# Optimization experiments

Hardware: AMD Instinct MI355X
Metric: run time of the kernel (lower is better)

The kernel has to match this reference:

```python
import jax, jax.numpy as jnp
import numpy as np

HIDDEN = 2048
NUM_HEADS = 16
NUM_KV_HEADS = 4
HEAD_DIM = HIDDEN // NUM_HEADS  # 128
ROPE_THETA = 1000000.0
B, S = 2, 2048


def setup_inputs() -> dict:
    key = jax.random.key(0)
    ks = jax.random.split(key, 10)
    sc = 0.02
    return {
        "hidden_states": jax.random.normal(ks[0], (B, S, HIDDEN), jnp.float32),
        "position_ids": jnp.broadcast_to(jnp.arange(S, dtype=jnp.int32), (B, S)),
        "Wq": jax.random.normal(ks[1], (HIDDEN, NUM_HEADS * HEAD_DIM), jnp.float32) * sc,
        "bq": jnp.zeros((NUM_HEADS * HEAD_DIM,), jnp.float32),
        "Wk": jax.random.normal(ks[2], (HIDDEN, NUM_KV_HEADS * HEAD_DIM), jnp.float32) * sc,
        "bk": jnp.zeros((NUM_KV_HEADS * HEAD_DIM,), jnp.float32),
        "Wv": jax.random.normal(ks[3], (HIDDEN, NUM_KV_HEADS * HEAD_DIM), jnp.float32) * sc,
        "bv": jnp.zeros((NUM_KV_HEADS * HEAD_DIM,), jnp.float32),
        "Wo": jax.random.normal(ks[4], (NUM_HEADS * HEAD_DIM, HIDDEN), jnp.float32) * sc,
        "bo": jnp.zeros((HIDDEN,), jnp.float32),
    }


def _rope_cos_sin(position_ids, dtype):
    # inv_freq: [head_dim/2]
    inv_freq = 1.0 / (ROPE_THETA ** (jnp.arange(0, HEAD_DIM, 2, dtype=jnp.float32) / HEAD_DIM))
    freqs = position_ids.astype(jnp.float32)[:, :, None] * inv_freq[None, None, :]  # [B,S,d/2]
    emb = jnp.concatenate([freqs, freqs], axis=-1)  # [B,S,d]
    return jnp.cos(emb).astype(dtype), jnp.sin(emb).astype(dtype)


def _rotate_half(x):
    h = x.shape[-1] // 2
    return jnp.concatenate([-x[..., h:], x[..., :h]], axis=-1)


def _attention(hidden_states, position_ids, Wq, bq, Wk, bk, Wv, bv, Wo, bo):
    bsz, q_len, _ = hidden_states.shape
    q = (hidden_states @ Wq + bq).reshape(bsz, q_len, NUM_HEADS, HEAD_DIM).transpose(0, 2, 1, 3)
    k = (hidden_states @ Wk + bk).reshape(bsz, q_len, NUM_KV_HEADS, HEAD_DIM).transpose(0, 2, 1, 3)
    v = (hidden_states @ Wv + bv).reshape(bsz, q_len, NUM_KV_HEADS, HEAD_DIM).transpose(0, 2, 1, 3)

    cos, sin = _rope_cos_sin(position_ids, hidden_states.dtype)
    cos = cos[:, None, :, :]  # [B,1,S,d]
    sin = sin[:, None, :, :]
    q = q * cos + _rotate_half(q) * sin
    k = k * cos + _rotate_half(k) * sin

    # repeat_kv (GQA): [B,kvh,S,d] -> [B,H,S,d]
    n_rep = NUM_HEADS // NUM_KV_HEADS
    k = jnp.repeat(k, n_rep, axis=1)
    v = jnp.repeat(v, n_rep, axis=1)

    scale = 1.0 / jnp.sqrt(jnp.array(HEAD_DIM, hidden_states.dtype))
    scores = jnp.einsum('bhqd,bhkd->bhqk', q, k) * scale  # [B,H,S,S]
    causal = jnp.tril(jnp.ones((q_len, q_len), bool))
    scores = jnp.where(causal[None, None], scores, jnp.finfo(scores.dtype).min)
    probs = jax.nn.softmax(scores.astype(jnp.float32), axis=-1).astype(hidden_states.dtype)
    attn = jnp.einsum('bhqk,bhkd->bhqd', probs, v)
    attn = attn.transpose(0, 2, 1, 3).reshape(bsz, q_len, HIDDEN)
    return attn @ Wo + bo


def reference(hidden_states, position_ids, Wq, bq, Wk, bk, Wv, bv, Wo, bo):
    return _attention(hidden_states, position_ids, Wq, bq, Wk, bk, Wv, bv, Wo, bo)
```

## Files before the change

kernel.cpp:

```cpp
#include <hip/hip_runtime.h>
#include <cmath>

#define HIDDEN 2048
#define NH 16
#define NKV 4
#define HD 128
#define SEQ 2048
#define BATCH 2

typedef unsigned short ushort_t;
typedef short bf16x8 __attribute__((ext_vector_type(8)));
typedef float f32x4 __attribute__((ext_vector_type(4)));
typedef ushort_t u16x4 __attribute__((ext_vector_type(4)));

__device__ __forceinline__ ushort_t f2bf(float f) {
    union { float f; unsigned int u; } v; v.f = f;
    unsigned int r = v.u + 0x7fffu + ((v.u >> 16) & 1u);
    return (ushort_t)(r >> 16);
}
__device__ __forceinline__ ushort_t f2bf_trunc(float f) {
    union { float f; unsigned int u; } v; v.f = f;
    return (ushort_t)(v.u >> 16);
}

__device__ __forceinline__ f32x4 mfma16(bf16x8 a, bf16x8 b, f32x4 c) {
    return __builtin_amdgcn_mfma_f32_16x16x32_bf16(a, b, c, 0, 0, 0);
}

__device__ __forceinline__ void load_lds16(const void* g, void* l) {
    __builtin_amdgcn_global_load_lds((const __attribute__((address_space(1))) unsigned int*)g,
                                     (__attribute__((address_space(3))) unsigned int*)l,
                                     16, 0, 0);
}


__global__ __launch_bounds__(256) void convert_x(const float* __restrict__ x,
                                                 ushort_t* __restrict__ xb, int n4) {
    int g = blockIdx.x * 256 + threadIdx.x;
    if (g >= n4) return;
    float4 v = ((const float4*)x)[g];
    u16x4 o;
    o[0] = f2bf(v.x); o[1] = f2bf(v.y); o[2] = f2bf(v.z); o[3] = f2bf(v.w);
    ((u16x4*)xb)[g] = o;
}

__global__ __launch_bounds__(256) void transpose_w(const float* __restrict__ W,
                                                   ushort_t* __restrict__ WT, int K, int N) {
    __shared__ ushort_t T[64][72];
    const int n0 = blockIdx.x * 64, k0 = blockIdx.y * 64;
    const int t = threadIdx.x;
    for (int idx = t; idx < 64 * 16; idx += 256) {
        int r = idx >> 4, c4 = (idx & 15) << 2;
        float4 v = *(const float4*)&W[(size_t)(k0 + r) * N + n0 + c4];
        T[r][c4 + 0] = f2bf(v.x); T[r][c4 + 1] = f2bf(v.y);
        T[r][c4 + 2] = f2bf(v.z); T[r][c4 + 3] = f2bf(v.w);
    }
    __syncthreads();
    for (int idx = t; idx < 64 * 16; idx += 256) {
        int n = idx >> 4, kg = (idx & 15) << 2;
        u16x4 o;
        o[0] = T[kg + 0][n]; o[1] = T[kg + 1][n];
        o[2] = T[kg + 2][n]; o[3] = T[kg + 3][n];
        *(u16x4*)&WT[(size_t)(n0 + n) * K + k0 + kg] = o;
    }
}

template <int MODE>
__global__ __launch_bounds__(256) void gemm_bt(const ushort_t* __restrict__ A,
                                               const ushort_t* __restrict__ Bt,
                                               const float* __restrict__ bias,
                                               const float* __restrict__ bias2,
                                               void* __restrict__ out,
                                               void* __restrict__ out2,
                                               int M, int N, int K,
                                               const int* __restrict__ posids) {
    __shared__ __align__(16) ushort_t As[2][128 * 32];
    __shared__ __align__(16) ushort_t Bs[2][128 * 32];
    const int tid = threadIdx.x;
    const int w = tid >> 6, lane = tid & 63, quad = lane >> 4, l16 = lane & 15;
    const int m0 = blockIdx.y * 128, n0 = blockIdx.x * 128;

    f32x4 acc[2][8];
    for (int i = 0; i < 2; i++)
        for (int j = 0; j < 8; j++)
            for (int e = 0; e < 4; e++) acc[i][j][e] = 0.0f;

    const int rr = lane >> 2;
    const int gc8 = (((lane & 3) ^ ((lane >> 3) & 3)) << 3);
    const ushort_t* Ag = A + (size_t)(m0 + w * 32 + rr) * K + gc8;
    const ushort_t* Bg = Bt + (size_t)(n0 + w * 32 + rr) * K + gc8;
    ushort_t* Al0 = &As[0][(w * 32) * 32];
    ushort_t* Bl0 = &Bs[0][(w * 32) * 32];

    auto stage = [&](int bi, int k0) {
        const ushort_t* ag = Ag + k0;
        const ushort_t* bg = Bg + k0;
        ushort_t* la = Al0 + bi * 128 * 32;
        ushort_t* lb = Bl0 + bi * 128 * 32;
        load_lds16(ag, la);
        load_lds16(ag + (size_t)16 * K, la + 512);
        load_lds16(bg, lb);
        load_lds16(bg + (size_t)16 * K, lb + 512);
    };

    const int nk = K >> 5;
    const int rsw = ((l16 >> 1) & 3);
    stage(0, 0);
    __syncthreads();

    for (int ki = 0; ki < nk; ki++) {
        const int cur = ki & 1;
        if (ki + 1 < nk) stage(cur ^ 1, (ki + 1) << 5);
        const ushort_t* Ab = As[cur];
        const ushort_t* Bb = Bs[cur];
        bf16x8 af[2];
#pragma unroll
        for (int i = 0; i < 2; i++)
            af[i] = *(const bf16x8*)&Ab[(w * 32 + i * 16 + l16) * 32 + (quad ^ rsw) * 8];
#pragma unroll
        for (int j = 0; j < 8; j++) {
            bf16x8 bf = *(const bf16x8*)&Bb[(j * 16 + l16) * 32 + (quad ^ rsw) * 8];
#pragma unroll
            for (int i = 0; i < 2; i++) acc[i][j] = mfma16(af[i], bf, acc[i][j]);
        }
        __syncthreads();
    }

    if (MODE == 0) {
        float* O = (float*)out;
#pragma unroll
        for (int i = 0; i < 2; i++)
#pragma unroll
            for (int r = 0; r < 4; r++) {
                int row = m0 + w * 32 + i * 16 + quad * 4 + r;
#pragma unroll
                for (int j = 0; j < 8; j++) {
                    int col = n0 + j * 16 + l16;
                    O[(size_t)row * N + col] = acc[i][j][r] + bias[col];
                }
            }
    } else if (MODE == 1) {
        ushort_t* O = (ushort_t*)out;
        const int h = n0 >> 7;
        const float scale = 0.08838834764831845f;
#pragma unroll
        for (int i = 0; i < 2; i++)
#pragma unroll
            for (int r = 0; r < 4; r++) {
                int row = m0 + w * 32 + i * 16 + quad * 4 + r;
                int b = row >> 11, s = row & (SEQ - 1);
                float pos = (float)posids[row];
                size_t obase = ((size_t)(b * NH + h) * SEQ + s) * HD;
#pragma unroll
                for (int j = 0; j < 4; j++) {
                    int dl = j * 16 + l16;
                    float x1 = acc[i][j][r] + bias[n0 + dl];
                    float x2 = acc[i][j + 4][r] + bias[n0 + dl + 64];
                    float ang = pos * __expf(-0.21586735246819178f * (float)dl);
                    float sn, cs;
                    __sincosf(ang, &sn, &cs);
                    O[obase + dl]      = f2bf((x1 * cs - x2 * sn) * scale);
                    O[obase + dl + 64] = f2bf((x2 * cs + x1 * sn) * scale);
                }
            }
    } else {
        if (n0 < 512) {
            ushort_t* O = (ushort_t*)out;
            const int h = n0 >> 7;
#pragma unroll
            for (int i = 0; i < 2; i++)
#pragma unroll
                for (int r = 0; r < 4; r++) {
                    int row = m0 + w * 32 + i * 16 + quad * 4 + r;
                    int b = row >> 11, s = row & (SEQ - 1);
                    float pos = (float)posids[row];
                    size_t obase = ((size_t)(b * NKV + h) * SEQ + s) * HD;
#pragma unroll
                    for (int j = 0; j < 4; j++) {
                        int dl = j * 16 + l16;
                        float x1 = acc[i][j][r] + bias[n0 + dl];
                        float x2 = acc[i][j + 4][r] + bias[n0 + dl + 64];
                        float ang = pos * __expf(-0.21586735246819178f * (float)dl);
                        float sn, cs;
                        __sincosf(ang, &sn, &cs);
                        O[obase + dl]      = f2bf(x1 * cs - x2 * sn);
                        O[obase + dl + 64] = f2bf(x2 * cs + x1 * sn);
                    }
                }
        } else {
            ushort_t* O = (ushort_t*)out2;
            const int n0v = n0 - 512;
            const int h = n0v >> 7;
#pragma unroll
            for (int i = 0; i < 2; i++)
#pragma unroll
                for (int r = 0; r < 4; r++) {
                    int row = m0 + w * 32 + i * 16 + quad * 4 + r;
                    int b = row >> 11, s = row & (SEQ - 1);
#pragma unroll
                    for (int j = 0; j < 8; j++) {
                        int d = (n0v & 127) + j * 16 + l16;
                        float v = acc[i][j][r] + bias2[n0v + j * 16 + l16];
                        O[((size_t)(b * NKV + h) * HD + d) * SEQ + s] = f2bf(v);
                    }
                }
        }
    }
}

__global__ __launch_bounds__(256) void flash(const ushort_t* __restrict__ Qr,
                                             const ushort_t* __restrict__ Kr,
                                             const ushort_t* __restrict__ Vt,
                                             ushort_t* __restrict__ Attn) {
    __shared__ __align__(16) ushort_t Ksh[2 * 4 * 64 * 32];
    __shared__ __align__(16) ushort_t Vsh[2 * 2 * 128 * 32];
    __shared__ __align__(16) ushort_t Ps[4 * 16 * 72];
    const int tid = threadIdx.x;
    const int w = tid >> 6, lane = tid & 63, quad = lane >> 4, l16 = lane & 15;
    const int x = blockIdx.x, h = blockIdx.y, b = blockIdx.z;
    const int qt = b ? x : (gridDim.x - 1 - x);
    const int q0 = qt * 128;
    const int nkt = 2 * qt + 2;
    const int hkv = h >> 2;
    const ushort_t* Kg = Kr + ((size_t)(b * NKV + hkv) * SEQ) * HD;
    const ushort_t* Vg = Vt + ((size_t)(b * NKV + hkv) * HD) * SEQ;

    const int p = lane >> 2;
    const int gc8 = (((lane & 3) ^ ((lane >> 3) & 3)) << 3);
    const ushort_t* kst = Kg + (size_t)p * HD + w * 32 + gc8;
    const ushort_t* vst = Vg + (size_t)((w & 1) * 64 + p) * SEQ + (w >> 1) * 32 + gc8;
    ushort_t* ksl = Ksh + w * 2048;
    ushort_t* vsl = Vsh + (w >> 1) * 4096 + (w & 1) * 2048;

    auto stage = [&](int bi, int kv0) {
        const ushort_t* gk = kst + (size_t)kv0 * HD;
        ushort_t* lk = ksl + bi * 8192;
        load_lds16(gk, lk);
        load_lds16(gk + (size_t)16 * HD, lk + 512);
        load_lds16(gk + (size_t)32 * HD, lk + 1024);
        load_lds16(gk + (size_t)48 * HD, lk + 1536);
        const ushort_t* gv = vst + kv0;
        ushort_t* lv = vsl + bi * 8192;
        load_lds16(gv, lv);
        load_lds16(gv + (size_t)16 * SEQ, lv + 512);
        load_lds16(gv + (size_t)32 * SEQ, lv + 1024);
        load_lds16(gv + (size_t)48 * SEQ, lv + 1536);
    };

    bf16x8 aq[2][4];
#pragma unroll
    for (int st = 0; st < 2; st++) {
        const size_t qrow = ((size_t)(b * NH + h) * SEQ + q0 + st * 64 + w * 16 + l16) * HD;
#pragma unroll
        for (int kc = 0; kc < 4; kc++)
            aq[st][kc] = *(const bf16x8*)&Qr[qrow + kc * 32 + quad * 8];
    }

    f32x4 o[2][8];
#pragma unroll
    for (int st = 0; st < 2; st++)
#pragma unroll
        for (int j = 0; j < 8; j++)
#pragma unroll
            for (int e = 0; e < 4; e++) o[st][j][e] = 0.0f;
    f32x4 ls2[2];
#pragma unroll
    for (int st = 0; st < 2; st++)
        for (int e = 0; e < 4; e++) ls2[st][e] = 0.0f;
    bf16x8 ones;
#pragma unroll
    for (int e = 0; e < 8; e++) ones[e] = (short)0x3F80;

    ushort_t* Pw = &Ps[w * 16 * 72];
    const int rsw8 = ((l16 >> 1) & 3) << 3;

    stage(0, 0);
    __syncthreads();

    for (int kt = 0; kt < nkt; kt++) {
        const int kv0 = kt * 64;
        const int cur = kt & 1;
        if (kt + 1 < nkt) stage(cur ^ 1, kv0 + 64);

        const ushort_t* Kb = Ksh + cur * 8192;
        const ushort_t* Vb = Vsh + cur * 8192;

#pragma unroll
        for (int st = 0; st < 2; st++) {
            if (st == 0 && kt == 2 * qt + 1) continue;

            f32x4 sa[4];
#pragma unroll
            for (int nt = 0; nt < 4; nt++)
#pragma unroll
                for (int e = 0; e < 4; e++) sa[nt][e] = 0.0f;
#pragma unroll
            for (int kc = 0; kc < 4; kc++) {
#pragma unroll
                for (int nt = 0; nt < 4; nt++) {
                    bf16x8 bk = *(const bf16x8*)&Kb[kc * 2048 + nt * 512 + l16 * 32 +
                                                    ((quad * 8) ^ rsw8)];
                    sa[nt] = mfma16(aq[st][kc], bk, sa[nt]);
                }
            }

            if ((kt >> 1) == qt && (kt & 1) == st) {
#pragma unroll
                for (int nt = 0; nt < 4; nt++)
#pragma unroll
                    for (int r = 0; r < 4; r++) {
                        int kvg = kv0 + nt * 16 + l16;
                        int qg = q0 + st * 64 + w * 16 + quad * 4 + r;
                        if (kvg > qg) sa[nt][r] = -1e30f;
                    }
            }

#pragma unroll
            for (int nt = 0; nt < 4; nt++)
#pragma unroll
                for (int r = 0; r < 4; r++)
                    Pw[(quad * 4 + r) * 72 + nt * 16 + l16] = f2bf_trunc(__expf(sa[nt][r]));

#pragma unroll
            for (int kc = 0; kc < 2; kc++) {
                bf16x8 ap = *(const bf16x8*)&Pw[l16 * 72 + kc * 32 + quad * 8];
                ls2[st] = mfma16(ap, ones, ls2[st]);
#pragma unroll
                for (int j = 0; j < 8; j++) {
                    bf16x8 bv = *(const bf16x8*)&Vb[kc * 4096 + (j * 16 + l16) * 32 +
                                                    ((quad * 8) ^ rsw8)];
                    o[st][j] = mfma16(ap, bv, o[st][j]);
                }
            }
        }
        __syncthreads();
    }

#pragma unroll
    for (int st = 0; st < 2; st++)
#pragma unroll
        for (int r = 0; r < 4; r++) {
            float inv = 1.0f / ls2[st][r];
            int row = b * SEQ + q0 + st * 64 + w * 16 + quad * 4 + r;
            size_t obase = (size_t)row * HIDDEN + h * HD;
#pragma unroll
            for (int j = 0; j < 8; j++) Attn[obase + j * 16 + l16] = f2bf(o[st][j][r] * inv);
        }
}

extern "C" void kernel_launch(void* const* d_in, const int* in_sizes, int n_in,
                              void* d_out, int out_size, void* d_ws, size_t ws_size,
                              hipStream_t stream) {
    const float* hs = (const float*)d_in[0];
    const int* posids = (const int*)d_in[1];
    const float* Wq = (const float*)d_in[2];
    const float* bq = (const float*)d_in[3];
    const float* Wk = (const float*)d_in[4];
    const float* bk = (const float*)d_in[5];
    const float* Wv = (const float*)d_in[6];
    const float* bv = (const float*)d_in[7];
    const float* Wo = (const float*)d_in[8];
    const float* bo = (const float*)d_in[9];
    float* out = (float*)d_out;

    char* ws = (char*)d_ws;
    size_t off = 0;
    auto alloc = [&](size_t bytes) {
        char* p = ws + off;
        off += (bytes + 255) & ~(size_t)255;
        return p;
    };
    ushort_t* Xb   = (ushort_t*)alloc(4096ull * 2048 * 2);
    ushort_t* WqT  = (ushort_t*)alloc(2048ull * 2048 * 2);
    ushort_t* WkvT = (ushort_t*)alloc(1024ull * 2048 * 2);
    ushort_t* WoT  = (ushort_t*)alloc(2048ull * 2048 * 2);
    ushort_t* Qr   = (ushort_t*)alloc((size_t)BATCH * NH * SEQ * HD * 2);
    ushort_t* Kr   = (ushort_t*)alloc((size_t)BATCH * NKV * SEQ * HD * 2);
    ushort_t* Vtr  = (ushort_t*)alloc((size_t)BATCH * NKV * HD * SEQ * 2);
    ushort_t* Attn = (ushort_t*)alloc(4096ull * 2048 * 2);

    convert_x<<<4096 * 2048 / 4 / 256, 256, 0, stream>>>(hs, Xb, 4096 * 2048 / 4);
    transpose_w<<<dim3(2048 / 64, 2048 / 64), 256, 0, stream>>>(Wq, WqT, 2048, 2048);
    transpose_w<<<dim3(512 / 64, 2048 / 64), 256, 0, stream>>>(Wk, WkvT, 2048, 512);
    transpose_w<<<dim3(512 / 64, 2048 / 64), 256, 0, stream>>>(Wv, WkvT + 512ull * 2048, 2048, 512);
    transpose_w<<<dim3(2048 / 64, 2048 / 64), 256, 0, stream>>>(Wo, WoT, 2048, 2048);

    gemm_bt<1><<<dim3(16, 32), 256, 0, stream>>>(Xb, WqT, bq, nullptr, Qr, nullptr,
                                                 4096, 2048, 2048, posids);
    gemm_bt<4><<<dim3(8, 32), 256, 0, stream>>>(Xb, WkvT, bk, bv, Kr, Vtr,
                                                4096, 1024, 2048, posids);

    flash<<<dim3(SEQ / 128, NH, BATCH), 256, 0, stream>>>(Qr, Kr, Vtr, Attn);

    gemm_bt<0><<<dim3(16, 32), 256, 0, stream>>>(Attn, WoT, bo, nullptr, out, nullptr,
                                                 4096, 2048, 2048, nullptr);
}
```

Baseline: 361.9 us.

## Fuse QKV projections into one GEMM, merge weight transposes, deepen output GEMM K-tile

Merges the four weight-transpose launches into one 3D-grid kernel and concatenates Wq/Wk/Wv into one transposed matrix. A single GEMM then computes Q, K and V, with the epilogue routed by column range. The output projection GEMM gains a templated K-tile of 64, staging two 32-wide chunks per barrier. This cuts launch count, balances waves across CUs, and halves barriers in the output GEMM, at the cost of doubled LDS use there.

```diff
diff --git a/kernel.cpp b/kernel.cpp
--- a/kernel.cpp
+++ b/kernel.cpp
@@ -44,10 +44,24 @@
     ((u16x4*)xb)[g] = o;
 }
 
-__global__ __launch_bounds__(256) void transpose_w(const float* __restrict__ W,
-                                                   ushort_t* __restrict__ WT, int K, int N) {
+__global__ __launch_bounds__(256) void transpose_all(const float* __restrict__ Wq,
+                                                     const float* __restrict__ Wk,
+                                                     const float* __restrict__ Wv,
+                                                     const float* __restrict__ Wo,
+                                                     ushort_t* __restrict__ WqkvT,
+                                                     ushort_t* __restrict__ WoT) {
+    const int z = blockIdx.z;
+    const float* W;
+    ushort_t* WT;
+    int N;
+    if (z == 0)      { W = Wq; WT = WqkvT;                        N = 2048; }
+    else if (z == 1) { W = Wk; WT = WqkvT + 2048ull * 2048;       N = 512;  }
+    else if (z == 2) { W = Wv; WT = WqkvT + 2560ull * 2048;       N = 512;  }
+    else             { W = Wo; WT = WoT;                          N = 2048; }
+    const int K = 2048;
+    const int n0 = blockIdx.x * 64, k0 = blockIdx.y * 64;
+    if (n0 >= N) return;
     __shared__ ushort_t T[64][72];
-    const int n0 = blockIdx.x * 64, k0 = blockIdx.y * 64;
     const int t = threadIdx.x;
     for (int idx = t; idx < 64 * 16; idx += 256) {
         int r = idx >> 4, c4 = (idx & 15) << 2;
@@ -65,17 +79,20 @@
     }
 }
 
-template <int MODE>
+template <int MODE, int BK>
 __global__ __launch_bounds__(256) void gemm_bt(const ushort_t* __restrict__ A,
                                                const ushort_t* __restrict__ Bt,
                                                const float* __restrict__ bias,
                                                const float* __restrict__ bias2,
+                                               const float* __restrict__ bias3,
                                                void* __restrict__ out,
                                                void* __restrict__ out2,
+                                               void* __restrict__ out3,
                                                int M, int N, int K,
                                                const int* __restrict__ posids) {
-    __shared__ __align__(16) ushort_t As[2][128 * 32];
-    __shared__ __align__(16) ushort_t Bs[2][128 * 32];
+    constexpr int CH = BK / 32;
+    __shared__ __align__(16) ushort_t As[2 * CH * 4096];
+    __shared__ __align__(16) ushort_t Bs[2 * CH * 4096];
     const int tid = threadIdx.x;
     const int w = tid >> 6, lane = tid & 63, quad = lane >> 4, l16 = lane & 15;
     const int m0 = blockIdx.y * 128, n0 = blockIdx.x * 128;
@@ -89,39 +106,45 @@
     const int gc8 = (((lane & 3) ^ ((lane >> 3) & 3)) << 3);
     const ushort_t* Ag = A + (size_t)(m0 + w * 32 + rr) * K + gc8;
     const ushort_t* Bg = Bt + (size_t)(n0 + w * 32 + rr) * K + gc8;
-    ushort_t* Al0 = &As[0][(w * 32) * 32];
-    ushort_t* Bl0 = &Bs[0][(w * 32) * 32];
+    ushort_t* Asw = As + w * 1024;
+    ushort_t* Bsw = Bs + w * 1024;
 
     auto stage = [&](int bi, int k0) {
-        const ushort_t* ag = Ag + k0;
-        const ushort_t* bg = Bg + k0;
-        ushort_t* la = Al0 + bi * 128 * 32;
-        ushort_t* lb = Bl0 + bi * 128 * 32;
-        load_lds16(ag, la);
-        load_lds16(ag + (size_t)16 * K, la + 512);
-        load_lds16(bg, lb);
-        load_lds16(bg + (size_t)16 * K, lb + 512);
+#pragma unroll
+        for (int kc = 0; kc < CH; kc++) {
+            const ushort_t* ag = Ag + k0 + kc * 32;
+            const ushort_t* bg = Bg + k0 + kc * 32;
+            ushort_t* la = Asw + (bi * CH + kc) * 4096;
+            ushort_t* lb = Bsw + (bi * CH + kc) * 4096;
+            load_lds16(ag, la);
+            load_lds16(ag + (size_t)16 * K, la + 512);
+            load_lds16(bg, lb);
+            load_lds16(bg + (size_t)16 * K, lb + 512);
+        }
     };
 
-    const int nk = K >> 5;
+    const int nk = K / BK;
     const int rsw = ((l16 >> 1) & 3);
     stage(0, 0);
     __syncthreads();
 
     for (int ki = 0; ki < nk; ki++) {
         const int cur = ki & 1;
-        if (ki + 1 < nk) stage(cur ^ 1, (ki + 1) << 5);
-        const ushort_t* Ab = As[cur];
-        const ushort_t* Bb = Bs[cur];
-        bf16x8 af[2];
-#pragma unroll
-        for (int i = 0; i < 2; i++)
-            af[i] = *(const bf16x8*)&Ab[(w * 32 + i * 16 + l16) * 32 + (quad ^ rsw) * 8];
-#pragma unroll
-        for (int j = 0; j < 8; j++) {
-            bf16x8 bf = *(const bf16x8*)&Bb[(j * 16 + l16) * 32 + (quad ^ rsw) * 8];
-#pragma unroll
-            for (int i = 0; i < 2; i++) acc[i][j] = mfma16(af[i], bf, acc[i][j]);
+        if (ki + 1 < nk) stage(cur ^ 1, (ki + 1) * BK);
+#pragma unroll
+        for (int kc = 0; kc < CH; kc++) {
+            const ushort_t* Ab = &As[(cur * CH + kc) * 4096];
+            const ushort_t* Bb = &Bs[(cur * CH + kc) * 4096];
+            bf16x8 af[2];
+#pragma unroll
+            for (int i = 0; i < 2; i++)
+                af[i] = *(const bf16x8*)&Ab[(w * 32 + i * 16 + l16) * 32 + (quad ^ rsw) * 8];
+#pragma unroll
+            for (int j = 0; j < 8; j++) {
+                bf16x8 bf = *(const bf16x8*)&Bb[(j * 16 + l16) * 32 + (quad ^ rsw) * 8];
+#pragma unroll
+                for (int i = 0; i < 2; i++) acc[i][j] = mfma16(af[i], bf, acc[i][j]);
+            }
         }
         __syncthreads();
     }
@@ -139,34 +162,11 @@
                     O[(size_t)row * N + col] = acc[i][j][r] + bias[col];
                 }
             }
-    } else if (MODE == 1) {
-        ushort_t* O = (ushort_t*)out;
-        const int h = n0 >> 7;
-        const float scale = 0.08838834764831845f;
-#pragma unroll
-        for (int i = 0; i < 2; i++)
-#pragma unroll
-            for (int r = 0; r < 4; r++) {
-                int row = m0 + w * 32 + i * 16 + quad * 4 + r;
-                int b = row >> 11, s = row & (SEQ - 1);
-                float pos = (float)posids[row];
-                size_t obase = ((size_t)(b * NH + h) * SEQ + s) * HD;
-#pragma unroll
-                for (int j = 0; j < 4; j++) {
-                    int dl = j * 16 + l16;
-                    float x1 = acc[i][j][r] + bias[n0 + dl];
-                    float x2 = acc[i][j + 4][r] + bias[n0 + dl + 64];
-                    float ang = pos * __expf(-0.21586735246819178f * (float)dl);
-                    float sn, cs;
-                    __sincosf(ang, &sn, &cs);
-                    O[obase + dl]      = f2bf((x1 * cs - x2 * sn) * scale);
-                    O[obase + dl + 64] = f2bf((x2 * cs + x1 * sn) * scale);
-                }
-            }
     } else {
-        if (n0 < 512) {
+        if (n0 < 2048) {
             ushort_t* O = (ushort_t*)out;
             const int h = n0 >> 7;
+            const float scale = 0.08838834764831845f;
 #pragma unroll
             for (int i = 0; i < 2; i++)
 #pragma unroll
@@ -174,7 +174,7 @@
                     int row = m0 + w * 32 + i * 16 + quad * 4 + r;
                     int b = row >> 11, s = row & (SEQ - 1);
                     float pos = (float)posids[row];
-                    size_t obase = ((size_t)(b * NKV + h) * SEQ + s) * HD;
+                    size_t obase = ((size_t)(b * NH + h) * SEQ + s) * HD;
 #pragma unroll
                     for (int j = 0; j < 4; j++) {
                         int dl = j * 16 + l16;
@@ -183,13 +183,37 @@
                         float ang = pos * __expf(-0.21586735246819178f * (float)dl);
                         float sn, cs;
                         __sincosf(ang, &sn, &cs);
+                        O[obase + dl]      = f2bf((x1 * cs - x2 * sn) * scale);
+                        O[obase + dl + 64] = f2bf((x2 * cs + x1 * sn) * scale);
+                    }
+                }
+        } else if (n0 < 2560) {
+            ushort_t* O = (ushort_t*)out2;
+            const int n0k = n0 - 2048;
+            const int h = n0k >> 7;
+#pragma unroll
+            for (int i = 0; i < 2; i++)
+#pragma unroll
+                for (int r = 0; r < 4; r++) {
+                    int row = m0 + w * 32 + i * 16 + quad * 4 + r;
+                    int b = row >> 11, s = row & (SEQ - 1);
+                    float pos = (float)posids[row];
+                    size_t obase = ((size_t)(b * NKV + h) * SEQ + s) * HD;
+#pragma unroll
+                    for (int j = 0; j < 4; j++) {
+                        int dl = j * 16 + l16;
+                        float x1 = acc[i][j][r] + bias2[n0k + dl];
+                        float x2 = acc[i][j + 4][r] + bias2[n0k + dl + 64];
+                        float ang = pos * __expf(-0.21586735246819178f * (float)dl);
+                        float sn, cs;
+                        __sincosf(ang, &sn, &cs);
                         O[obase + dl]      = f2bf(x1 * cs - x2 * sn);
                         O[obase + dl + 64] = f2bf(x2 * cs + x1 * sn);
                     }
                 }
         } else {
-            ushort_t* O = (ushort_t*)out2;
-            const int n0v = n0 - 512;
+            ushort_t* O = (ushort_t*)out3;
+            const int n0v = n0 - 2560;
             const int h = n0v >> 7;
 #pragma unroll
             for (int i = 0; i < 2; i++)
@@ -199,8 +223,8 @@
                     int b = row >> 11, s = row & (SEQ - 1);
 #pragma unroll
                     for (int j = 0; j < 8; j++) {
-                        int d = (n0v & 127) + j * 16 + l16;
-                        float v = acc[i][j][r] + bias2[n0v + j * 16 + l16];
+                        int d = j * 16 + l16;
+                        float v = acc[i][j][r] + bias3[n0v + d];
                         O[((size_t)(b * NKV + h) * HD + d) * SEQ + s] = f2bf(v);
                     }
                 }
@@ -370,28 +394,22 @@
         off += (bytes + 255) & ~(size_t)255;
         return p;
     };
-    ushort_t* Xb   = (ushort_t*)alloc(4096ull * 2048 * 2);
-    ushort_t* WqT  = (ushort_t*)alloc(2048ull * 2048 * 2);
-    ushort_t* WkvT = (ushort_t*)alloc(1024ull * 2048 * 2);
-    ushort_t* WoT  = (ushort_t*)alloc(2048ull * 2048 * 2);
-    ushort_t* Qr   = (ushort_t*)alloc((size_t)BATCH * NH * SEQ * HD * 2);
-    ushort_t* Kr   = (ushort_t*)alloc((size_t)BATCH * NKV * SEQ * HD * 2);
-    ushort_t* Vtr  = (ushort_t*)alloc((size_t)BATCH * NKV * HD * SEQ * 2);
-    ushort_t* Attn = (ushort_t*)alloc(4096ull * 2048 * 2);
+    ushort_t* Xb     = (ushort_t*)alloc(4096ull * 2048 * 2);
+    ushort_t* WqkvT  = (ushort_t*)alloc(3072ull * 2048 * 2);
+    ushort_t* WoT    = (ushort_t*)alloc(2048ull * 2048 * 2);
+    ushort_t* Qr     = (ushort_t*)alloc((size_t)BATCH * NH * SEQ * HD * 2);
+    ushort_t* Kr     = (ushort_t*)alloc((size_t)BATCH * NKV * SEQ * HD * 2);
+    ushort_t* Vtr    = (ushort_t*)alloc((size_t)BATCH * NKV * HD * SEQ * 2);
+    ushort_t* Attn   = (ushort_t*)alloc(4096ull * 2048 * 2);
 
     convert_x<<<4096 * 2048 / 4 / 256, 256, 0, stream>>>(hs, Xb, 4096 * 2048 / 4);
-    transpose_w<<<dim3(2048 / 64, 2048 / 64), 256, 0, stream>>>(Wq, WqT, 2048, 2048);
-    transpose_w<<<dim3(512 / 64, 2048 / 64), 256, 0, stream>>>(Wk, WkvT, 2048, 512);
-    transpose_w<<<dim3(512 / 64, 2048 / 64), 256, 0, stream>>>(Wv, WkvT + 512ull * 2048, 2048, 512);
-    transpose_w<<<dim3(2048 / 64, 2048 / 64), 256, 0, stream>>>(Wo, WoT, 2048, 2048);
-
-    gemm_bt<1><<<dim3(16, 32), 256, 0, stream>>>(Xb, WqT, bq, nullptr, Qr, nullptr,
-                                                 4096, 2048, 2048, posids);
-    gemm_bt<4><<<dim3(8, 32), 256, 0, stream>>>(Xb, WkvT, bk, bv, Kr, Vtr,
-                                                4096, 1024, 2048, posids);
+    transpose_all<<<dim3(32, 32, 4), 256, 0, stream>>>(Wq, Wk, Wv, Wo, WqkvT, WoT);
+
+    gemm_bt<2, 32><<<dim3(24, 32), 256, 0, stream>>>(Xb, WqkvT, bq, bk, bv,
+                                                     Qr, Kr, Vtr, 4096, 3072, 2048, posids);
 
     flash<<<dim3(SEQ / 128, NH, BATCH), 256, 0, stream>>>(Qr, Kr, Vtr, Attn);
 
-    gemm_bt<0><<<dim3(16, 32), 256, 0, stream>>>(Attn, WoT, bo, nullptr, out, nullptr,
-                                                 4096, 2048, 2048, nullptr);
-}
+    gemm_bt<0, 64><<<dim3(16, 32), 256, 0, stream>>>(Attn, WoT, bo, nullptr, nullptr,
+                                                     out, nullptr, nullptr, 4096, 2048, 2048, nullptr);
+}
```

Result: faster. 348.2 us (-3.8%).
